# Performance work log

Hardware: AMD Instinct MI355X
Metric: run time of the kernel (lower is better)

The kernel has to match this reference:

```python
import jax, jax.numpy as jnp
from jax import lax
import numpy as np

N_DIMS, HGT, WID = 256, 32, 32
D_STATE, D_CONV, EXPAND = 64, 4, 2
D_INNER = EXPAND * N_DIMS          # 512
DT_RANK = (N_DIMS + 15) // 16      # 16


def setup_inputs() -> dict:
    key = jax.random.key(0)
    ks = jax.random.split(key, 14)
    s = 0.02
    return {
        "x": jax.random.normal(ks[0], (16, N_DIMS, HGT, WID), jnp.float32),
        "rel_h": jax.random.normal(ks[1], (1, N_DIMS, 1, HGT), jnp.float32),
        "rel_w": jax.random.normal(ks[2], (1, N_DIMS, WID, 1), jnp.float32),
        "gate_w": jax.random.normal(ks[3], (N_DIMS, N_DIMS, 3), jnp.float32) * s,
        "gate_b": jnp.zeros((N_DIMS,), jnp.float32),
        "in_proj_w": jax.random.normal(ks[4], (2 * D_INNER, N_DIMS), jnp.float32) * s,
        "conv_w": jax.random.normal(ks[5], (D_INNER, 1, D_CONV), jnp.float32) * 0.2,
        "conv_b": jnp.zeros((D_INNER,), jnp.float32),
        "x_proj_w": jax.random.normal(ks[6], (DT_RANK + 2 * D_STATE, D_INNER), jnp.float32) * s,
        "dt_proj_w": jax.random.normal(ks[7], (D_INNER, DT_RANK), jnp.float32) * s,
        "dt_proj_b": jax.random.normal(ks[8], (D_INNER,), jnp.float32) * 0.1,
        "A_log": jnp.log(jnp.tile(jnp.arange(1, D_STATE + 1, dtype=jnp.float32)[None, :], (D_INNER, 1))),
        "D": jnp.ones((D_INNER,), jnp.float32),
        "out_proj_w": jax.random.normal(ks[9], (N_DIMS, D_INNER), jnp.float32) * s,
    }


def _forward(x, rel_h, rel_w, gate_w, gate_b, in_proj_w, conv_w, conv_b,
             x_proj_w, dt_proj_w, dt_proj_b, A_log, D, out_proj_w):
    B, C, H, W = x.shape
    L = H * W
    xs = x.reshape(B, C, L).transpose(0, 2, 1)                      # (B,L,C)
    pos = (rel_h + rel_w).reshape(1, C, L).transpose(0, 2, 1)       # (1,L,C)
    xs = xs + pos

    # Conv1d(C,C,k=3,pad=1) + sigmoid gate on channel-first layout
    xp = xs.transpose(0, 2, 1)                                      # (B,C,L)
    ctx = jax.nn.sigmoid(
        lax.conv_general_dilated(xp, gate_w, (1,), [(1, 1)],
                                 dimension_numbers=("NCH", "OIH", "NCH"))
        + gate_b[None, :, None]
    ).transpose(0, 2, 1)                                            # (B,L,C)

    # ---- Mamba block ----
    xz = xs @ in_proj_w.T                                           # (B,L,2*d_inner)
    u, z = jnp.split(xz, 2, axis=-1)
    # depthwise causal conv (d_conv=4): left-pad 3
    uc = lax.conv_general_dilated(u.transpose(0, 2, 1), conv_w, (1,), [(D_CONV - 1, 0)],
                                  dimension_numbers=("NCH", "OIH", "NCH"),
                                  feature_group_count=D_INNER) + conv_b[None, :, None]
    u = jax.nn.silu(uc).transpose(0, 2, 1)                          # (B,L,d_inner)

    x_dbl = u @ x_proj_w.T                                          # (B,L,dt_rank+2n)
    dt, Bm, Cm = jnp.split(x_dbl, [DT_RANK, DT_RANK + D_STATE], axis=-1)
    delta = jax.nn.softplus(dt @ dt_proj_w.T + dt_proj_b)           # (B,L,d_inner)
    A = -jnp.exp(A_log)                                             # (d_inner,n)

    def step(h, inp):
        d_t, B_t, C_t, u_t = inp                                    # (B,d)(B,n)(B,n)(B,d)
        dA = jnp.exp(d_t[..., None] * A)                            # (B,d,n)
        h = dA * h + (d_t * u_t)[..., None] * B_t[:, None, :]
        y = jnp.einsum("bdn,bn->bd", h, C_t)
        return h, y

    h0 = jnp.zeros((B, D_INNER, D_STATE), u.dtype)
    _, ys = lax.scan(step, h0, (delta.transpose(1, 0, 2), Bm.transpose(1, 0, 2),
                                Cm.transpose(1, 0, 2), u.transpose(1, 0, 2)))
    y = ys.transpose(1, 0, 2) + u * D                               # (B,L,d_inner)
    y = y * jax.nn.silu(z)
    x_mamba = y @ out_proj_w.T                                      # (B,L,C)

    # contiguous-memory view(B,C,H,W) in torch == plain reshape of (B,L,C)
    return (x_mamba * ctx).reshape(B, C, H, W)


def reference(x, rel_h, rel_w, gate_w, gate_b, in_proj_w, conv_w, conv_b,
              x_proj_w, dt_proj_w, dt_proj_b, A_log, D, out_proj_w):
    return _forward(x, rel_h, rel_w, gate_w, gate_b, in_proj_w, conv_w, conv_b,
                    x_proj_w, dt_proj_w, dt_proj_b, A_log, D, out_proj_w)
```

## Files before the change

kernel.cpp:

```cpp
#include <hip/hip_runtime.h>
#include <hip/hip_fp16.h>
#include <math.h>

#define NB 16
#define NC 256
#define NL 1024
#define NDI 512
#define NCH 32
#define CH 32
#define MTOT (NB*NL)

typedef __attribute__((ext_vector_type(8))) short s8b;
typedef __attribute__((ext_vector_type(4))) float f4;
typedef __attribute__((ext_vector_type(2))) float f2;
typedef unsigned short ushort_t;

__device__ __forceinline__ float sigmoidf_(float x){ return 1.f/(1.f+__expf(-x)); }

__device__ __forceinline__ ushort2 split2(float f){
  unsigned u = __float_as_uint(f);
  unsigned hi = (u + 0x7fffu + ((u>>16)&1u)) & 0xffff0000u;
  float rem = f - __uint_as_float(hi);
  unsigned ur = __float_as_uint(rem);
  unsigned lo = (ur + 0x7fffu + ((ur>>16)&1u)) >> 16;
  ushort2 r; r.x = (ushort_t)(hi>>16); r.y = (ushort_t)lo; return r;
}
__device__ __forceinline__ float b2f(ushort_t h){ return __uint_as_float(((unsigned)h)<<16); }

__global__ void split_w_k(const float* __restrict__ W, ushort_t* __restrict__ hi,
                          ushort_t* __restrict__ lo, int n){
  int i = blockIdx.x*256 + threadIdx.x;
  if (i < n) { ushort2 s = split2(W[i]); hi[i] = s.x; lo[i] = s.y; }
}
__global__ void split_gw_k(const float* __restrict__ gw, ushort_t* __restrict__ hi,
                           ushort_t* __restrict__ lo){
  int idx = blockIdx.x*256 + threadIdx.x;
  if (idx >= 256*768) return;
  int co = idx / 768, k = idx % 768;
  int tap = k >> 8, ci = k & 255;
  ushort2 s = split2(gw[co*768 + ci*3 + tap]);
  hi[idx] = s.x; lo[idx] = s.y;
}

__global__ __launch_bounds__(256) void k0_xs(const float* __restrict__ x,
                                             const float* __restrict__ rel_h,
                                             const float* __restrict__ rel_w,
                                             ushort_t* __restrict__ xs_hi,
                                             ushort_t* __restrict__ xs_lo){
  __shared__ float tile[32][33];
  int b = blockIdx.z, c0 = blockIdx.y*32, l0 = blockIdx.x*32;
  int tid = threadIdx.x;
  int j = tid & 31, i0 = tid >> 5;
#pragma unroll
  for (int r = 0; r < 4; ++r) {
    int i = i0 + r*8;
    tile[i][j] = x[((size_t)(b*NC + c0 + i))*NL + l0 + j];
  }
  __syncthreads();
  int cl = tid & 31, lq = tid >> 5;
#pragma unroll
  for (int r = 0; r < 4; ++r) {
    int ll = lq + r*8;
    int l = l0 + ll, c = c0 + cl;
    float v = tile[cl][ll] + rel_h[c*32 + (l & 31)] + rel_w[c*32 + (l >> 5)];
    ushort2 s = split2(v);
    size_t o = ((size_t)(b*NL + l))*NC + c;
    xs_hi[o] = s.x; xs_lo[o] = s.y;
  }
}

enum { EPI_STORE=0, EPI_SPLIT=1, EPI_SIGB=2, EPI_MUL=3 };

template<int EPI, bool CONVA>
__global__ __launch_bounds__(256) void mgemm_k(
    const ushort_t* __restrict__ Ahp, const ushort_t* __restrict__ Alp,
    const ushort_t* __restrict__ Bhp, const ushort_t* __restrict__ Blp,
    const float* __restrict__ bias, const float* __restrict__ aux,
    float* __restrict__ out0, float* __restrict__ out1,
    ushort_t* __restrict__ ohi, ushort_t* __restrict__ olo,
    int N, int K, int AK)
{
  __shared__ ushort_t Ah[128][40], Al[128][40];
  const int tid = threadIdx.x;
  const int m0 = blockIdx.y * 128, n0 = blockIdx.x * 64;
  const int w = tid >> 6, l = tid & 63;
  const int wr = (w >> 1) * 64, wc = (w & 1) * 32;
  const int l15 = l & 15, lk = l >> 4;
  const int ar = tid >> 1, ak = (tid & 1) * 16;
  f4 acc[4][2] = {};

  int bn0 = n0 + wc + l15;        if (bn0 >= N) bn0 = N-1;
  int bn1 = n0 + wc + 16 + l15;   if (bn1 >= N) bn1 = N-1;
  const size_t brow0 = (size_t)bn0 * K, brow1 = (size_t)bn1 * K;

  for (int k0 = 0; k0 < K; k0 += 32) {
    {
      uint4 h0 = {0,0,0,0}, h1 = {0,0,0,0}, l0v = {0,0,0,0}, l1v = {0,0,0,0};
      long srow = m0 + ar; int scol = k0 + ak;
      bool v = true;
      if (CONVA) {
        int tap = k0 >> 8;
        int lpos = ((m0 + ar) & (NL-1)) + tap - 1;
        v = (unsigned)lpos < (unsigned)NL;
        srow = (long)(m0 + ar) + tap - 1;
        scol = (k0 & 255) + ak;
      }
      if (v) {
        const ushort_t* sh = Ahp + (size_t)srow * AK + scol;
        const ushort_t* sl = Alp + (size_t)srow * AK + scol;
        h0  = *(const uint4*)(sh);     h1  = *(const uint4*)(sh + 8);
        l0v = *(const uint4*)(sl);     l1v = *(const uint4*)(sl + 8);
      }
      *(uint4*)&Ah[ar][ak]   = h0;  *(uint4*)&Ah[ar][ak+8] = h1;
      *(uint4*)&Al[ar][ak]   = l0v; *(uint4*)&Al[ar][ak+8] = l1v;
    }
    const int kb = k0 + lk*8;
    s8b bh0 = *(const s8b*)(Bhp + brow0 + kb);
    s8b bl0 = *(const s8b*)(Blp + brow0 + kb);
    s8b bh1 = *(const s8b*)(Bhp + brow1 + kb);
    s8b bl1 = *(const s8b*)(Blp + brow1 + kb);
    __syncthreads();
    s8b afh[4], afl[4];
#pragma unroll
    for (int i = 0; i < 4; ++i) {
      afh[i] = *(const s8b*)&Ah[wr + i*16 + l15][lk*8];
      afl[i] = *(const s8b*)&Al[wr + i*16 + l15][lk*8];
    }
#pragma unroll
    for (int i = 0; i < 4; ++i) {
      acc[i][0] = __builtin_amdgcn_mfma_f32_16x16x32_bf16(afh[i], bh0, acc[i][0], 0, 0, 0);
      acc[i][0] = __builtin_amdgcn_mfma_f32_16x16x32_bf16(afl[i], bh0, acc[i][0], 0, 0, 0);
      acc[i][0] = __builtin_amdgcn_mfma_f32_16x16x32_bf16(afh[i], bl0, acc[i][0], 0, 0, 0);
      acc[i][1] = __builtin_amdgcn_mfma_f32_16x16x32_bf16(afh[i], bh1, acc[i][1], 0, 0, 0);
      acc[i][1] = __builtin_amdgcn_mfma_f32_16x16x32_bf16(afl[i], bh1, acc[i][1], 0, 0, 0);
      acc[i][1] = __builtin_amdgcn_mfma_f32_16x16x32_bf16(afh[i], bl1, acc[i][1], 0, 0, 0);
    }
    __syncthreads();
  }

#pragma unroll
  for (int i = 0; i < 4; ++i) {
#pragma unroll
    for (int j = 0; j < 2; ++j) {
#pragma unroll
      for (int r = 0; r < 4; ++r) {
        int m = m0 + wr + i*16 + lk*4 + r;
        int n = n0 + wc + j*16 + l15;
        float v = acc[i][j][r];
        if (EPI == EPI_STORE) {
          if (n < N) out0[(size_t)m*N + n] = v;
        } else if (EPI == EPI_SPLIT) {
          if (n < NDI) { ushort2 s = split2(v); ohi[(size_t)m*NDI + n] = s.x; olo[(size_t)m*NDI + n] = s.y; }
          else out0[(size_t)m*NDI + n - NDI] = v;
        } else if (EPI == EPI_SIGB) {
          out0[(size_t)m*N + n] = sigmoidf_(v + bias[n]);
        } else {
          out0[(size_t)m*N + n] = v * aux[(size_t)m*N + n];
        }
      }
    }
  }
}

__global__ __launch_bounds__(256) void k3_dwconv(const ushort_t* __restrict__ u_hi,
                                                 const ushort_t* __restrict__ u_lo,
                                                 const float* __restrict__ cw,
                                                 const float* __restrict__ cb,
                                                 ushort_t* __restrict__ up_hi,
                                                 ushort_t* __restrict__ up_lo){
  int idx = blockIdx.x*256 + threadIdx.x;
  int d8 = idx & (NDI/8 - 1);
  int bl = idx >> 6;
  int l = bl & (NL-1);
  int d0 = d8*8;
  float a[8];
#pragma unroll
  for (int j = 0; j < 8; ++j) a[j] = cb[d0+j];
#pragma unroll
  for (int t = 0; t < 4; ++t) {
    int lp = l - 3 + t;
    if (lp >= 0) {
      size_t o = (size_t)(bl - 3 + t)*NDI + d0;
      uint4 ph = *reinterpret_cast<const uint4*>(&u_hi[o]);
      uint4 pl = *reinterpret_cast<const uint4*>(&u_lo[o]);
      const unsigned* hw = &ph.x; const unsigned* lw = &pl.x;
#pragma unroll
      for (int q = 0; q < 4; ++q) {
        float v0 = b2f((ushort_t)(hw[q] & 0xffffu)) + b2f((ushort_t)(lw[q] & 0xffffu));
        float v1 = b2f((ushort_t)(hw[q] >> 16))     + b2f((ushort_t)(lw[q] >> 16));
        a[q*2+0] += v0 * cw[(d0+q*2+0)*4 + t];
        a[q*2+1] += v1 * cw[(d0+q*2+1)*4 + t];
      }
    }
  }
  uint4 oh, ol;
  unsigned* ohw = &oh.x; unsigned* olw = &ol.x;
#pragma unroll
  for (int q = 0; q < 4; ++q) {
    float f0 = a[q*2+0] * sigmoidf_(a[q*2+0]);
    float f1 = a[q*2+1] * sigmoidf_(a[q*2+1]);
    ushort2 s0 = split2(f0), s1 = split2(f1);
    ohw[q] = (unsigned)s0.x | ((unsigned)s1.x << 16);
    olw[q] = (unsigned)s0.y | ((unsigned)s1.y << 16);
  }
  size_t o = (size_t)bl*NDI + d0;
  *reinterpret_cast<uint4*>(&up_hi[o]) = oh;
  *reinterpret_cast<uint4*>(&up_lo[o]) = ol;
}

__global__ __launch_bounds__(256,4) void scan_a(
    const float* __restrict__ xdbl,
    const ushort_t* __restrict__ up_hi, const ushort_t* __restrict__ up_lo,
    const float* __restrict__ dtw, const float* __restrict__ dtb,
    const float* __restrict__ Dvec,
    float* __restrict__ cdbuf, float* __restrict__ ylocal,
    __half* __restrict__ hend, float* __restrict__ cdsum)
{
  __shared__ float bs[CH][64];
  __shared__ float cs[CH][64];
  __shared__ float dts[CH][16];
  const int tid = threadIdx.x;
  const int b = blockIdx.z, c = blockIdx.y;
  const int wv = tid >> 6, lane = tid & 63;
  const int sub = lane >> 5;
  const int dl0 = lane & 31;
  const int d = blockIdx.x*128 + wv*32 + dl0;
  const int nb = sub*32;
  const int rowbase = b*NL + c*CH;
  for (int i = tid; i < CH*128; i += 256) {
    int t = i >> 7, cc = i & 127;
    float v = xdbl[(size_t)(rowbase + t)*144 + 16 + cc];
    if (cc < 64) bs[t][cc] = v; else cs[t][cc-64] = v;
  }
  for (int i = tid; i < CH*16; i += 256) {
    int t = i >> 4, r = i & 15;
    dts[t][r] = xdbl[(size_t)(rowbase + t)*144 + r];
  }
  __syncthreads();

  f2 w2[8];
  {
    const f2* wp = reinterpret_cast<const f2*>(dtw + d*16);
#pragma unroll
    for (int r = 0; r < 8; ++r) w2[r] = wp[r];
  }
  const float bia = dtb[d];
  const float Dd = Dvec[d];

  f2 h2[16];
#pragma unroll
  for (int n = 0; n < 16; ++n) h2[n] = (f2){0.f, 0.f};
  float cd = 0.f;
  const size_t base = (size_t)rowbase*NDI + d;

  for (int t = 0; t < CH; ++t) {
    const size_t off = base + (size_t)t*NDI;
    f2 dd = (f2){bia, 0.f};
    const f2* dt2 = reinterpret_cast<const f2*>(&dts[t][0]);
#pragma unroll
    for (int g = 0; g < 8; ++g) dd = dd + dt2[g]*w2[g];
    float dacc = dd.x + dd.y;
    float e   = __expf(dacc);
    float r   = 1.f/(1.f+e);
    float dlv = (dacc > 20.f) ? dacc : -__logf(r);
    float uu = b2f(up_hi[off]) + b2f(up_lo[off]);
    cd += dlv;
    float du = dlv*uu;
    float r2 = r*r, r4 = r2*r2;
    float r8 = r4*r4, r16 = r8*r8, r32 = r16*r16;
    const f2 du2 = (f2){du, du};
    const f2 rp  = (f2){r,  r2};
    const f2 rq  = (f2){r2, r2};
    const f2 r4v = (f2){r4, r4};
    f2 mb2 = sub ? (f2){r32, r32} : (f2){1.f, 1.f};
    f2 yacc = (f2){sub ? 0.f : uu*Dd, 0.f};
#pragma unroll
    for (int g = 0; g < 8; ++g) {
      float4 B4 = *reinterpret_cast<const float4*>(&bs[t][nb + g*4]);
      float4 C4 = *reinterpret_cast<const float4*>(&cs[t][nb + g*4]);
      f2 B01 = (f2){B4.x, B4.y}, B23 = (f2){B4.z, B4.w};
      f2 C01 = (f2){C4.x, C4.y}, C23 = (f2){C4.z, C4.w};
      f2 p01 = mb2 * rp;
      f2 p23 = p01 * rq;
      mb2 = mb2 * r4v;
      h2[g*2+0] = p01*h2[g*2+0] + du2*B01;
      h2[g*2+1] = p23*h2[g*2+1] + du2*B23;
      yacc = yacc + h2[g*2+0]*C01;
      yacc = yacc + h2[g*2+1]*C23;
    }
    float acc = yacc.x + yacc.y;
    acc += __shfl_xor(acc, 32, 64);
    if (sub == 0) {
      cdbuf[off] = cd;
      ylocal[off] = acc;
    }
  }
  if (sub == 0) cdsum[(size_t)(b*NCH+c)*NDI + d] = cd;
  const size_t hb = ((size_t)(b*NCH+c)*64 + nb)*NDI + d;
#pragma unroll
  for (int n = 0; n < 16; ++n) {
    hend[hb + (size_t)(2*n  )*NDI] = __float2half(h2[n].x);
    hend[hb + (size_t)(2*n+1)*NDI] = __float2half(h2[n].y);
  }
}

__global__ __launch_bounds__(256) void scan_b(
    __half* __restrict__ hend, const float* __restrict__ cdsum)
{
  int gid = blockIdx.x*256 + threadIdx.x;
  int d = gid & 511;
  int n = (gid >> 9) & 63;
  int b = gid >> 15;
  float h = 0.f;
  const float npow = (float)(n+1);
  for (int c = 0; c < NCH; ++c) {
    size_t hi = ((size_t)((b*NCH+c)*64+n))*NDI + d;
    float he  = __half2float(hend[hi]);
    float cdv = cdsum[(size_t)(b*NCH+c)*NDI + d];
    hend[hi] = __float2half(h);
    h = __expf(-npow*cdv)*h + he;
  }
}

__global__ __launch_bounds__(256,4) void scan_c(
    const float* __restrict__ cdbuf, const float* __restrict__ zbuf,
    const float* __restrict__ xdbl, const __half* __restrict__ hin,
    const float* __restrict__ ylocal,
    ushort_t* __restrict__ y_hi, ushort_t* __restrict__ y_lo)
{
  __shared__ float cs[CH][64];
  const int tid = threadIdx.x;
  const int b = blockIdx.z, c = blockIdx.y;
  const int wv = tid >> 6, lane = tid & 63;
  const int sub = lane >> 5;
  const int dl0 = lane & 31;
  const int d = blockIdx.x*128 + wv*32 + dl0;
  const int nb = sub*32;
  const int rowbase = b*NL + c*CH;
  for (int i = tid; i < CH*64; i += 256) {
    int t = i >> 6, n = i & 63;
    cs[t][n] = xdbl[(size_t)(rowbase + t)*144 + 80 + n];
  }
  __syncthreads();

  f2 q2[16];
  if (c > 0) {
    const size_t hb = ((size_t)(b*NCH+c)*64 + nb)*NDI + d;
#pragma unroll
    for (int n = 0; n < 16; ++n) {
      q2[n].x = __half2float(hin[hb + (size_t)(2*n  )*NDI]);
      q2[n].y = __half2float(hin[hb + (size_t)(2*n+1)*NDI]);
    }
  } else {
#pragma unroll
    for (int n = 0; n < 16; ++n) q2[n] = (f2){0.f, 0.f};
  }
  const size_t base = (size_t)rowbase*NDI + d;
  for (int t = 0; t < CH; ++t) {
    const size_t off = base + (size_t)t*NDI;
    float cdv = cdbuf[off];
    float rt = __expf(-cdv);
    float r2 = rt*rt, r4 = r2*r2;
    float r8 = r4*r4, r16 = r8*r8, r32 = r16*r16;
    const f2 rp  = (f2){rt, r2};
    const f2 rq  = (f2){r2, r2};
    const f2 r4v = (f2){r4, r4};
    f2 mb2 = sub ? (f2){r32, r32} : (f2){1.f, 1.f};
    f2 yacc = (f2){0.f, 0.f};
#pragma unroll
    for (int g = 0; g < 8; ++g) {
      float4 C4 = *reinterpret_cast<const float4*>(&cs[t][nb + g*4]);
      f2 C01 = (f2){C4.x, C4.y}, C23 = (f2){C4.z, C4.w};
      f2 p01 = mb2 * rp;
      f2 p23 = p01 * rq;
      mb2 = mb2 * r4v;
      yacc = yacc + p01*(q2[g*2+0]*C01);
      yacc = yacc + p23*(q2[g*2+1]*C23);
    }
    float acc = yacc.x + yacc.y;
    acc += __shfl_xor(acc, 32, 64);
    if (sub == 0) {
      float zv  = zbuf[off];
      float yv  = ylocal[off] + acc;
      float fin = yv * (zv * sigmoidf_(zv));
      ushort2 s = split2(fin);
      y_hi[off] = s.x; y_lo[off] = s.y;
    }
  }
}

extern "C" void kernel_launch(void* const* d_in, const int* in_sizes, int n_in,
                              void* d_out, int out_size, void* d_ws, size_t ws_size,
                              hipStream_t stream)
{
  const float* x      = (const float*)d_in[0];
  const float* rel_h  = (const float*)d_in[1];
  const float* rel_w  = (const float*)d_in[2];
  const float* gate_w = (const float*)d_in[3];
  const float* gate_b = (const float*)d_in[4];
  const float* ipw    = (const float*)d_in[5];
  const float* conv_w = (const float*)d_in[6];
  const float* conv_b = (const float*)d_in[7];
  const float* xpw    = (const float*)d_in[8];
  const float* dtw    = (const float*)d_in[9];
  const float* dtb    = (const float*)d_in[10];
  const float* A_log  = (const float*)d_in[11]; (void)A_log;
  const float* Dv     = (const float*)d_in[12];
  const float* opw    = (const float*)d_in[13];

  float* ws = (float*)d_ws;
  float*    ctx   = ws;
  ushort_t* u_hi  = (ushort_t*)(ws + 4194304);
  ushort_t* u_lo  = (ushort_t*)(ws + 8388608);
  float*    ylocal= ws + 4194304;
  float*    zbuf  = ws + 12582912;
  ushort_t* up_hi = (ushort_t*)(ws + 20971520);
  ushort_t* up_lo = (ushort_t*)(ws + 25165824);
  ushort_t* y_hi  = up_hi;
  ushort_t* y_lo  = up_lo;
  float*    xdbl  = ws + 29360128;
  float*    cdbuf = ws + 31719424;
  float*    cdsum = ws + 40108032;
  ushort_t* gw_hi = (ushort_t*)(ws + 40370176);
  ushort_t* gw_lo = (ushort_t*)(ws + 40468480);
  ushort_t* ip_hi = (ushort_t*)(ws + 40566784);
  ushort_t* ip_lo = (ushort_t*)(ws + 40697856);
  ushort_t* xp_hi = (ushort_t*)(ws + 40828928);
  ushort_t* xp_lo = (ushort_t*)(ws + 40865792);
  ushort_t* op_hi = (ushort_t*)(ws + 40902656);
  ushort_t* op_lo = (ushort_t*)(ws + 40968192);
  __half*   hend  = (__half*)(ws + 41033728);
  ushort_t* xs_hi = (ushort_t*)(ws + 41033728);
  ushort_t* xs_lo = (ushort_t*)(ws + 43130880);

  split_gw_k<<<768, 256, 0, stream>>>(gate_w, gw_hi, gw_lo);
  split_w_k<<<1024, 256, 0, stream>>>(ipw, ip_hi, ip_lo, 262144);
  split_w_k<<<288, 256, 0, stream>>>(xpw, xp_hi, xp_lo, 73728);
  split_w_k<<<512, 256, 0, stream>>>(opw, op_hi, op_lo, 131072);

  k0_xs<<<dim3(32,8,16), 256, 0, stream>>>(x, rel_h, rel_w, xs_hi, xs_lo);

  mgemm_k<EPI_SIGB, true><<<dim3(4, 128), 256, 0, stream>>>(
      xs_hi, xs_lo, gw_hi, gw_lo, gate_b, nullptr, ctx, nullptr, nullptr, nullptr,
      256, 768, 256);

  mgemm_k<EPI_SPLIT, false><<<dim3(16, 128), 256, 0, stream>>>(
      xs_hi, xs_lo, ip_hi, ip_lo, nullptr, nullptr, zbuf, nullptr, u_hi, u_lo,
      1024, 256, 256);

  k3_dwconv<<<(NB*NL*NDI/8)/256, 256, 0, stream>>>(u_hi, u_lo, conv_w, conv_b, up_hi, up_lo);

  mgemm_k<EPI_STORE, false><<<dim3(3, 128), 256, 0, stream>>>(
      up_hi, up_lo, xp_hi, xp_lo, nullptr, nullptr, xdbl, nullptr, nullptr, nullptr,
      144, 512, 512);

  scan_a<<<dim3(4, NCH, NB), 256, 0, stream>>>(xdbl, up_hi, up_lo, dtw, dtb, Dv,
                                               cdbuf, ylocal, hend, cdsum);
  scan_b<<<(NB*64*NDI)/256, 256, 0, stream>>>(hend, cdsum);
  scan_c<<<dim3(4, NCH, NB), 256, 0, stream>>>(cdbuf, zbuf, xdbl, hend, ylocal, y_hi, y_lo);

  mgemm_k<EPI_MUL, false><<<dim3(4, 128), 256, 0, stream>>>(
      y_hi, y_lo, op_hi, op_lo, nullptr, ctx, (float*)d_out, nullptr, nullptr, nullptr,
      256, 512, 512);
}
```

Measured before the change: 426.3 us.

## Stage GEMM B tiles in LDS and recompute cumulative delta in scan_c

The GEMM kernel now loads B-operand hi/lo tiles cooperatively into shared memory instead of each wave fetching its own fragments from global memory. The scan also stops writing and re-reading a full per-token cumulative-delta buffer; scan_c recomputes delta from the dt projection and keeps a running product of exp(-delta). This trades about 64MB of global traffic for extra arithmetic and adds LDS pressure in the GEMM. The running product may accumulate rounding differently from the original exp of the sum.

```diff
diff --git a/kernel.cpp b/kernel.cpp
--- a/kernel.cpp
+++ b/kernel.cpp
@@ -80,18 +80,15 @@
     ushort_t* __restrict__ ohi, ushort_t* __restrict__ olo,
     int N, int K, int AK)
 {
-  __shared__ ushort_t Ah[128][40], Al[128][40];
+  __shared__ ushort_t Ah[128][40], Al[128][40], Bh[64][40], Bl[64][40];
   const int tid = threadIdx.x;
   const int m0 = blockIdx.y * 128, n0 = blockIdx.x * 64;
   const int w = tid >> 6, l = tid & 63;
   const int wr = (w >> 1) * 64, wc = (w & 1) * 32;
   const int l15 = l & 15, lk = l >> 4;
   const int ar = tid >> 1, ak = (tid & 1) * 16;
+  const int br = (tid & 127) >> 1;
   f4 acc[4][2] = {};
-
-  int bn0 = n0 + wc + l15;        if (bn0 >= N) bn0 = N-1;
-  int bn1 = n0 + wc + 16 + l15;   if (bn1 >= N) bn1 = N-1;
-  const size_t brow0 = (size_t)bn0 * K, brow1 = (size_t)bn1 * K;
 
   for (int k0 = 0; k0 < K; k0 += 32) {
     {
@@ -114,11 +111,17 @@
       *(uint4*)&Ah[ar][ak]   = h0;  *(uint4*)&Ah[ar][ak+8] = h1;
       *(uint4*)&Al[ar][ak]   = l0v; *(uint4*)&Al[ar][ak+8] = l1v;
     }
-    const int kb = k0 + lk*8;
-    s8b bh0 = *(const s8b*)(Bhp + brow0 + kb);
-    s8b bl0 = *(const s8b*)(Blp + brow0 + kb);
-    s8b bh1 = *(const s8b*)(Bhp + brow1 + kb);
-    s8b bl1 = *(const s8b*)(Blp + brow1 + kb);
+    {
+      uint4 p0 = {0,0,0,0}, p1 = {0,0,0,0};
+      int n = n0 + br;
+      const ushort_t* srcB = (tid < 128 ? Bhp : Blp);
+      if (n < N) {
+        const ushort_t* s = srcB + (size_t)n * K + k0 + ak;
+        p0 = *(const uint4*)(s); p1 = *(const uint4*)(s + 8);
+      }
+      if (tid < 128) { *(uint4*)&Bh[br][ak] = p0; *(uint4*)&Bh[br][ak+8] = p1; }
+      else           { *(uint4*)&Bl[br][ak] = p0; *(uint4*)&Bl[br][ak+8] = p1; }
+    }
     __syncthreads();
     s8b afh[4], afl[4];
 #pragma unroll
@@ -127,13 +130,15 @@
       afl[i] = *(const s8b*)&Al[wr + i*16 + l15][lk*8];
     }
 #pragma unroll
-    for (int i = 0; i < 4; ++i) {
-      acc[i][0] = __builtin_amdgcn_mfma_f32_16x16x32_bf16(afh[i], bh0, acc[i][0], 0, 0, 0);
-      acc[i][0] = __builtin_amdgcn_mfma_f32_16x16x32_bf16(afl[i], bh0, acc[i][0], 0, 0, 0);
-      acc[i][0] = __builtin_amdgcn_mfma_f32_16x16x32_bf16(afh[i], bl0, acc[i][0], 0, 0, 0);
-      acc[i][1] = __builtin_amdgcn_mfma_f32_16x16x32_bf16(afh[i], bh1, acc[i][1], 0, 0, 0);
-      acc[i][1] = __builtin_amdgcn_mfma_f32_16x16x32_bf16(afl[i], bh1, acc[i][1], 0, 0, 0);
-      acc[i][1] = __builtin_amdgcn_mfma_f32_16x16x32_bf16(afh[i], bl1, acc[i][1], 0, 0, 0);
+    for (int j = 0; j < 2; ++j) {
+      s8b bh = *(const s8b*)&Bh[wc + j*16 + l15][lk*8];
+      s8b bl = *(const s8b*)&Bl[wc + j*16 + l15][lk*8];
+#pragma unroll
+      for (int i = 0; i < 4; ++i) {
+        acc[i][j] = __builtin_amdgcn_mfma_f32_16x16x32_bf16(afh[i], bh, acc[i][j], 0, 0, 0);
+        acc[i][j] = __builtin_amdgcn_mfma_f32_16x16x32_bf16(afl[i], bh, acc[i][j], 0, 0, 0);
+        acc[i][j] = __builtin_amdgcn_mfma_f32_16x16x32_bf16(afh[i], bl, acc[i][j], 0, 0, 0);
+      }
     }
     __syncthreads();
   }
@@ -213,7 +218,7 @@
     const ushort_t* __restrict__ up_hi, const ushort_t* __restrict__ up_lo,
     const float* __restrict__ dtw, const float* __restrict__ dtb,
     const float* __restrict__ Dvec,
-    float* __restrict__ cdbuf, float* __restrict__ ylocal,
+    float* __restrict__ ylocal,
     __half* __restrict__ hend, float* __restrict__ cdsum)
 {
   __shared__ float bs[CH][64];
@@ -290,10 +295,7 @@
     }
     float acc = yacc.x + yacc.y;
     acc += __shfl_xor(acc, 32, 64);
-    if (sub == 0) {
-      cdbuf[off] = cd;
-      ylocal[off] = acc;
-    }
+    if (sub == 0) ylocal[off] = acc;
   }
   if (sub == 0) cdsum[(size_t)(b*NCH+c)*NDI + d] = cd;
   const size_t hb = ((size_t)(b*NCH+c)*64 + nb)*NDI + d;
@@ -323,12 +325,13 @@
 }
 
 __global__ __launch_bounds__(256,4) void scan_c(
-    const float* __restrict__ cdbuf, const float* __restrict__ zbuf,
-    const float* __restrict__ xdbl, const __half* __restrict__ hin,
-    const float* __restrict__ ylocal,
+    const float* __restrict__ xdbl, const float* __restrict__ zbuf,
+    const __half* __restrict__ hin, const float* __restrict__ ylocal,
+    const float* __restrict__ dtw, const float* __restrict__ dtb,
     ushort_t* __restrict__ y_hi, ushort_t* __restrict__ y_lo)
 {
   __shared__ float cs[CH][64];
+  __shared__ float dts[CH][16];
   const int tid = threadIdx.x;
   const int b = blockIdx.z, c = blockIdx.y;
   const int wv = tid >> 6, lane = tid & 63;
@@ -341,7 +344,19 @@
     int t = i >> 6, n = i & 63;
     cs[t][n] = xdbl[(size_t)(rowbase + t)*144 + 80 + n];
   }
+  for (int i = tid; i < CH*16; i += 256) {
+    int t = i >> 4, r = i & 15;
+    dts[t][r] = xdbl[(size_t)(rowbase + t)*144 + r];
+  }
   __syncthreads();
+
+  f2 w2[8];
+  {
+    const f2* wp = reinterpret_cast<const f2*>(dtw + d*16);
+#pragma unroll
+    for (int r = 0; r < 8; ++r) w2[r] = wp[r];
+  }
+  const float bia = dtb[d];
 
   f2 q2[16];
   if (c > 0) {
@@ -356,10 +371,16 @@
     for (int n = 0; n < 16; ++n) q2[n] = (f2){0.f, 0.f};
   }
   const size_t base = (size_t)rowbase*NDI + d;
+  float rt = 1.f;
   for (int t = 0; t < CH; ++t) {
     const size_t off = base + (size_t)t*NDI;
-    float cdv = cdbuf[off];
-    float rt = __expf(-cdv);
+    f2 dd = (f2){bia, 0.f};
+    const f2* dt2 = reinterpret_cast<const f2*>(&dts[t][0]);
+#pragma unroll
+    for (int g = 0; g < 8; ++g) dd = dd + dt2[g]*w2[g];
+    float dacc = dd.x + dd.y;
+    float e = __expf(dacc);
+    rt *= 1.f/(1.f+e);
     float r2 = rt*rt, r4 = r2*r2;
     float r8 = r4*r4, r16 = r8*r8, r32 = r16*r16;
     const f2 rp  = (f2){rt, r2};
@@ -419,7 +440,6 @@
   ushort_t* y_hi  = up_hi;
   ushort_t* y_lo  = up_lo;
   float*    xdbl  = ws + 29360128;
-  float*    cdbuf = ws + 31719424;
   float*    cdsum = ws + 40108032;
   ushort_t* gw_hi = (ushort_t*)(ws + 40370176);
   ushort_t* gw_lo = (ushort_t*)(ws + 40468480);
@@ -455,9 +475,9 @@
       144, 512, 512);
 
   scan_a<<<dim3(4, NCH, NB), 256, 0, stream>>>(xdbl, up_hi, up_lo, dtw, dtb, Dv,
-                                               cdbuf, ylocal, hend, cdsum);
+                                               ylocal, hend, cdsum);
   scan_b<<<(NB*64*NDI)/256, 256, 0, stream>>>(hend, cdsum);
-  scan_c<<<dim3(4, NCH, NB), 256, 0, stream>>>(cdbuf, zbuf, xdbl, hend, ylocal, y_hi, y_lo);
+  scan_c<<<dim3(4, NCH, NB), 256, 0, stream>>>(xdbl, zbuf, hend, ylocal, dtw, dtb, y_hi, y_lo);
 
   mgemm_k<EPI_MUL, false><<<dim3(4, 128), 256, 0, stream>>>(
       y_hi, y_lo, op_hi, op_lo, nullptr, ctx, (float*)d_out, nullptr, nullptr, nullptr,
```

Result: no change. 421.8 us (-1.1%).
